# Optimization experiments

Hardware: AMD Instinct MI355X
Metric: run time of the kernel (lower is better)

Reference implementation:

```python
import jax, jax.numpy as jnp
import numpy as np

B, N, F, H1, H2, NC = 1024, 64, 1024, 256, 128, 128
ALPHA = 0.2   # LeakyReLU slope
BN_EPS = 1e-5


def setup_inputs() -> dict:
    key = jax.random.key(0)
    ks = jax.random.split(key, 20)
    d = {}
    d["x"] = jax.random.normal(ks[0], (B, 1, F), dtype=jnp.float32)
    d["neighbor"] = jax.random.normal(ks[1], (B, N, 1, F), dtype=jnp.float32)
    # GraphAttn layer 1 params
    d["W1"] = jax.random.normal(ks[2], (H1, F), dtype=jnp.float32) / np.sqrt(F)
    d["b1"] = jnp.zeros((H1,), dtype=jnp.float32)
    d["a11"] = jax.random.normal(ks[3], (H1,), dtype=jnp.float32) / np.sqrt(H1)
    d["a12"] = jax.random.normal(ks[4], (H1,), dtype=jnp.float32) / np.sqrt(H1)
    d["g1"] = jnp.ones((), dtype=jnp.float32)   # BatchNorm1d(1) weight (scalar)
    d["be1"] = jnp.zeros((), dtype=jnp.float32)  # BatchNorm1d(1) bias
    # GraphAttn layer 2 params
    d["W2"] = jax.random.normal(ks[5], (H2, H1), dtype=jnp.float32) / np.sqrt(H1)
    d["b2"] = jnp.zeros((H2,), dtype=jnp.float32)
    d["a21"] = jax.random.normal(ks[6], (H2,), dtype=jnp.float32) / np.sqrt(H2)
    d["a22"] = jax.random.normal(ks[7], (H2,), dtype=jnp.float32) / np.sqrt(H2)
    d["g2"] = jnp.ones((), dtype=jnp.float32)
    d["be2"] = jnp.zeros((), dtype=jnp.float32)
    # final classifier
    d["Wl"] = jax.random.normal(ks[8], (NC, H2), dtype=jnp.float32) / np.sqrt(H2)
    d["bl"] = jnp.zeros((NC,), dtype=jnp.float32)
    return d


def _l2norm_c(t):
    # torch nf.normalize default: p=2, dim=1 -> here the singleton channel axis (-2)
    n = jnp.sqrt(jnp.sum(t * t, axis=-2, keepdims=True))
    return t / jnp.maximum(n, 1e-12)


def _gat_layer(x, nb, W, b, a_self, a_nb):
    # x: [B,1,Fin], nb: [B,N,1,Fin]
    xh = jnp.einsum('bcf,hf->bch', x, W) + b        # [B,1,H]
    nbh = jnp.einsum('bncf,hf->bnch', nb, W) + b    # [B,N,1,H]
    # att1(x[i]) + att2(neighbor[i]) -> scores over N (C==1 squeezed)
    s = (jnp.einsum('bch,h->bc', xh, a_self)[:, None, :]
         + jnp.einsum('bnch,h->bnc', nbh, a_nb))[..., 0]   # [B,N]
    A = jax.nn.softmax(jax.nn.leaky_relu(s, ALPHA), axis=1)  # softmax over neighbors
    out = jnp.einsum('bn,bnch->bch', A, nbh)        # [B,1,H]
    return out, nbh


def _bn_relu(t, g, b, axes):
    # BatchNorm1d(1) in training mode: stats over all non-channel dims of the tensor
    m = jnp.mean(t, axis=axes, keepdims=True)
    v = jnp.mean(jnp.square(t - m), axis=axes, keepdims=True)
    return jax.nn.relu(g * (t - m) * jax.lax.rsqrt(v + BN_EPS) + b)


def reference(x, neighbor, W1, b1, a11, a12, g1, be1,
              W2, b2, a21, a22, g2, be2, Wl, bl):
    x = _l2norm_c(x)
    nb = _l2norm_c(neighbor)
    x, nb = _gat_layer(x, nb, W1, b1, a11, a12)
    # acvt1 applied to x [B,1,H1] (stats over B,H) and to each neighbor tensor
    # [N,1,H1] separately (per-sample stats -> axes (1,3) of [B,N,1,H1])
    x = _bn_relu(x, g1, be1, axes=(0, 2))
    nb = _bn_relu(nb, g1, be1, axes=(1, 3))
    x, nb = _gat_layer(x, nb, W2, b2, a21, a22)
    x = _bn_relu(x, g2, be2, axes=(0, 2))
    # Flatten -> Dropout(p=0) -> Linear
    logits = jnp.einsum('bh,ch->bc', x.reshape(x.shape[0], -1), Wl) + bl
    return logits
```

## Files before the change

kernel.cpp:

```cpp
#include <hip/hip_runtime.h>
#include <hip/hip_bf16.h>
#include <stdint.h>

#define B_    1024
#define N_    64
#define F_    1024
#define H1_   256
#define H2_   128
#define NC_   128
#define ALPHA 0.2f
#define BN_EPS 1e-5f

typedef __attribute__((ext_vector_type(4))) float  f32x4;
typedef __attribute__((ext_vector_type(8))) __bf16 bf16x8;
typedef __attribute__((ext_vector_type(4))) __bf16 bf16x4;

__device__ inline float sign_ref(float v) {
    float s = copysignf(1.0f, v);
    return (fabsf(v) >= 1e-12f) ? s : v * 1e12f;
}

__device__ __forceinline__ void gload_lds16(const void* g, void* l) {
    auto gp = reinterpret_cast<const __attribute__((address_space(1))) void*>(
        reinterpret_cast<uintptr_t>(g));
    auto lp = reinterpret_cast<__attribute__((address_space(3))) void*>(
        reinterpret_cast<uintptr_t>(l));
    __builtin_amdgcn_global_load_lds(gp, lp, 16, 0, 0);
}

__device__ inline float blk_reduce(float v, float* buf) {
    #pragma unroll
    for (int o = 32; o > 0; o >>= 1) v += __shfl_xor(v, o, 64);
    __syncthreads();
    const int wave = threadIdx.x >> 6, lane = threadIdx.x & 63;
    if (lane == 0) buf[wave] = v;
    __syncthreads();
    float r = 0.f;
    if (threadIdx.x == 0) {
        const int nw = blockDim.x >> 6;
        for (int i = 0; i < nw; ++i) r += buf[i];
    }
    return r;
}

__global__ __launch_bounds__(256) void k_prep(
    const float* __restrict__ W1, const float* __restrict__ W2,
    const float* __restrict__ b1, const float* __restrict__ a11,
    const float* __restrict__ a12, const float* __restrict__ b2,
    const float* __restrict__ a21, const float* __restrict__ a22,
    __bf16* __restrict__ W1f, __bf16* __restrict__ W2b,
    float* __restrict__ w1a, float* __restrict__ w2a,
    float* __restrict__ w2a22, float* __restrict__ cscal)
{
    __shared__ float rbuf[8];
    const int blk = blockIdx.x, tid = threadIdx.x;
    if (blk < 256) {
        const int h = blk, k0 = tid * 4;
        float4 v = *(const float4*)(W1 + h * F_ + k0);
        bf16x4 p = { (__bf16)v.x, (__bf16)v.y, (__bf16)v.z, (__bf16)v.w };
        const int kc = k0 >> 5, kq = (k0 >> 3) & 3, j = k0 & 7;
        const int rbk = h >> 4, rowin = h & 15;
        *(bf16x4*)(W1f + (size_t)((kc * 16 + rbk) * 64 + kq * 16 + rowin) * 8 + j) = p;
    } else if (blk < 288) {
        const int i0 = (blk - 256) * 1024 + tid * 4;
        float4 v = *(const float4*)(W2 + i0);
        bf16x4 p = { (__bf16)v.x, (__bf16)v.y, (__bf16)v.z, (__bf16)v.w };
        *(bf16x4*)(W2b + i0) = p;
    } else if (blk < 292) {
        const int f = (blk - 288) * 256 + tid;
        float s1 = 0.f;
        #pragma unroll 8
        for (int h = 0; h < H1_; ++h) s1 += W1[h * F_ + f] * a11[h];
        w1a[f] = s1;
    } else if (blk == 292) {
        float s1 = 0.f, s2 = 0.f;
        #pragma unroll 8
        for (int h = 0; h < H2_; ++h) {
            const float w = W2[h * H1_ + tid];
            s1 += w * a21[h]; s2 += w * a22[h];
        }
        w2a[tid] = s1; w2a22[tid] = s2;
    } else {
        float v1 = b1[tid] * a11[tid];
        float v2 = (tid < H2_) ? b2[tid] * a21[tid] : 0.f;
        float v3 = (tid < H2_) ? b2[tid] * a22[tid] : 0.f;
        float r1 = blk_reduce(v1, rbuf);
        float r2 = blk_reduce(v2, rbuf);
        float r3 = blk_reduce(v3, rbuf);
        if (tid == 0) { cscal[0] = r1; cscal[1] = r2; cscal[2] = r3; }
    }
}

__global__ __launch_bounds__(256, 3) void k_gemm1(
    const float* __restrict__ A, const __bf16* __restrict__ Bw,
    const float* __restrict__ bias, __bf16* __restrict__ C,
    const float* __restrict__ x, const float* __restrict__ w1a,
    const float* __restrict__ a12, const float* __restrict__ w2a22,
    const float* __restrict__ cscal, const float* __restrict__ g1p,
    const float* __restrict__ be1p,
    float* __restrict__ out1, float* __restrict__ alpha1,
    float* __restrict__ beta1, float* __restrict__ psum1,
    float* __restrict__ psq1, float* __restrict__ spart)
{
    constexpr int K = F_;
    constexpr int LDA = 72;
    __shared__ __attribute__((aligned(16))) char smem[64 * 256 * 2];
    __bf16* As0 = (__bf16*)smem;
    __bf16* As1 = As0 + 64 * LDA;
    __bf16* Cs  = (__bf16*)smem;
    __shared__ float a12s[H1_];
    __shared__ float w2a22s[H1_];
    __shared__ float sv[N_];
    __shared__ float rbuf[8];
    __shared__ float fscal[4];

    const int tid = threadIdx.x;
    const int wave = tid >> 6, lane = tid & 63;
    const int rowin = lane & 15, kq = lane >> 4;
    const size_t b = blockIdx.x;

    {
        const float* xb = x + b * F_;
        float p0 = 0.f;
        #pragma unroll
        for (int i = 0; i < 4; ++i)
            p0 += sign_ref(xb[tid + i * 256]) * w1a[tid + i * 256];
        a12s[tid] = a12[tid]; w2a22s[tid] = w2a22[tid];
        float r0 = blk_reduce(p0, rbuf);
        if (tid == 0) fscal[0] = r0 + cscal[0];
    }

    f32x4 acc[4][4] = {};

    const int cqA = tid & 15, r0A = tid >> 4;
    const float* Abase = A + b * (size_t)64 * K + cqA * 4;

    auto mfma_phase = [&](const __bf16* buf, int kc0) {
        #pragma unroll
        for (int ks = 0; ks < 2; ++ks) {
            bf16x8 af[4], bv[4];
            #pragma unroll
            for (int mi = 0; mi < 4; ++mi)
                af[mi] = *(const bf16x8*)&buf[(mi * 16 + rowin) * LDA + ks * 32 + kq * 8];
            #pragma unroll
            for (int ni = 0; ni < 4; ++ni)
                bv[ni] = ((const bf16x8*)Bw)[((kc0 + ks) * 16 + wave * 4 + ni) * 64 + lane];
            #pragma unroll
            for (int mi = 0; mi < 4; ++mi)
                #pragma unroll
                for (int ni = 0; ni < 4; ++ni)
                    acc[mi][ni] = __builtin_amdgcn_mfma_f32_16x16x32_bf16(
                        af[mi], bv[ni], acc[mi][ni], 0, 0, 0);
        }
    };
    auto stage = [&](__bf16* buf, const float4* av) {
        #pragma unroll
        for (int rr = 0; rr < 4; ++rr) {
            const float4 v = av[rr];
            bf16x4 p = { (__bf16)sign_ref(v.x), (__bf16)sign_ref(v.y),
                         (__bf16)sign_ref(v.z), (__bf16)sign_ref(v.w) };
            *(bf16x4*)&buf[(r0A + rr * 16) * LDA + cqA * 4] = p;
        }
    };

    float4 avA[4], avB[4];
    #pragma unroll
    for (int rr = 0; rr < 4; ++rr)
        avA[rr] = *(const float4*)(Abase + (size_t)(r0A + rr * 16) * K);

    for (int kk = 0; kk < 8; ++kk) {
        const int k0 = kk * 128;
        #pragma unroll
        for (int rr = 0; rr < 4; ++rr)
            avB[rr] = *(const float4*)(Abase + (size_t)(r0A + rr * 16) * K + k0 + 64);
        stage(As0, avA);
        asm volatile("s_waitcnt lgkmcnt(0)" ::: "memory");
        __builtin_amdgcn_s_barrier();
        __builtin_amdgcn_sched_barrier(0);
        mfma_phase(As0, kk * 4);
        if (kk < 7) {
            #pragma unroll
            for (int rr = 0; rr < 4; ++rr)
                avA[rr] = *(const float4*)(Abase + (size_t)(r0A + rr * 16) * K + k0 + 128);
        }
        stage(As1, avB);
        asm volatile("s_waitcnt lgkmcnt(0)" ::: "memory");
        __builtin_amdgcn_s_barrier();
        __builtin_amdgcn_sched_barrier(0);
        mfma_phase(As1, kk * 4 + 2);
    }
    __syncthreads();

    const int cr0 = (lane >> 4) * 4, cc = lane & 15;
    #pragma unroll
    for (int ni = 0; ni < 4; ++ni) {
        const int col = wave * 64 + ni * 16 + cc;
        const float bs = bias[col];
        #pragma unroll
        for (int mi = 0; mi < 4; ++mi)
            #pragma unroll
            for (int i = 0; i < 4; ++i)
                Cs[(mi * 16 + cr0 + i) * 256 + col] = (__bf16)(acc[mi][ni][i] + bs);
    }
    __syncthreads();
    #pragma unroll
    for (int it = 0; it < 8; ++it) {
        const int s = it * 256 + tid;
        *(bf16x8*)(C + (b * 64 + (s >> 5)) * 256 + (s & 31) * 8) =
            *(const bf16x8*)&Cs[s * 8];
    }
    {
        const int n = tid >> 2, q = tid & 3;
        float p = 0.f;
        for (int i = 0; i < 64; ++i) {
            const int h = q * 64 + ((i + tid) & 63);
            p += (float)Cs[n * 256 + h] * a12s[h];
        }
        p += __shfl_xor(p, 1); p += __shfl_xor(p, 2);
        if (q == 0) { float s = fscal[0] + p; sv[n] = s > 0.f ? s : ALPHA * s; }
    }
    __syncthreads();
    if (tid < 64) {
        float s = sv[tid], m = s;
        #pragma unroll
        for (int o = 1; o < 64; o <<= 1) m = fmaxf(m, __shfl_xor(m, o));
        float e = __expf(s - m), t = e;
        #pragma unroll
        for (int o = 1; o < 64; o <<= 1) t += __shfl_xor(t, o);
        sv[tid] = e / t;
    }
    __syncthreads();
    float o1 = 0.f, ss = 0.f, sq = 0.f;
    for (int n2 = 0; n2 < N_; ++n2) {
        const float v = (float)Cs[n2 * 256 + tid];
        o1 += sv[n2] * v; ss += v; sq += v * v;
    }
    out1[b * H1_ + tid] = o1;
    {
        const float rs = blk_reduce(ss, rbuf);
        const float rq = blk_reduce(sq, rbuf);
        if (tid == 0) {
            const float inv = 1.f / (float)(N_ * H1_);
            const float mean = rs * inv, var = rq * inv - mean * mean;
            const float a = (*g1p) * rsqrtf(var + BN_EPS);
            const float bb = (*be1p) - a * mean;
            alpha1[b] = a; beta1[b] = bb;
            fscal[2] = a; fscal[3] = bb;
        }
        const float rsx = blk_reduce(o1, rbuf);
        const float rqx = blk_reduce(o1 * o1, rbuf);
        if (tid == 0) { psum1[b] = rsx; psq1[b] = rqx; }
    }
    __syncthreads();
    {
        const float al_ = fscal[2], be_ = fscal[3];
        const int n = tid >> 2, q = tid & 3;
        float p = 0.f;
        for (int i = 0; i < 64; ++i) {
            const int h = q * 64 + ((i + tid) & 63);
            const float v = (float)Cs[n * 256 + h];
            p += fmaxf(fmaf(al_, v, be_), 0.f) * w2a22s[h];
        }
        p += __shfl_xor(p, 1); p += __shfl_xor(p, 2);
        if (q == 0) spart[b * N_ + n] = p;
    }
}

__global__ __launch_bounds__(256) void k_back(
    const __bf16* __restrict__ nbh1, const float* __restrict__ out1,
    const float* __restrict__ alpha1, const float* __restrict__ beta1,
    const float* __restrict__ psum1, const float* __restrict__ psq1,
    const float* __restrict__ g1p, const float* __restrict__ be1p,
    const float* __restrict__ w2a, const float* __restrict__ spart,
    const float* __restrict__ cscal, const __bf16* __restrict__ W2b,
    const float* __restrict__ b2,
    float* __restrict__ out2, float* __restrict__ psum2,
    float* __restrict__ psq2)
{
    __shared__ __attribute__((aligned(16))) __bf16 tile[N_ * H1_];
    __shared__ float w2as[H1_];
    __shared__ float sv[N_];
    __shared__ float g2s[H1_ + 8];
    __shared__ float hpart[H2_];
    __shared__ float rbuf[8];
    __shared__ float scal[3];

    const int b = blockIdx.x, tid = threadIdx.x;

    const __bf16* src = nbh1 + (size_t)b * N_ * H1_;
    #pragma unroll
    for (int it = 0; it < 8; ++it)
        gload_lds16(src + (it * 256 + tid) * 8, tile + (it * 256 + tid) * 8);
    w2as[tid] = w2a[tid];
    const float o1 = out1[(size_t)b * H1_ + tid];
    const float al = alpha1[b], be = beta1[b];

    {
        float s = 0.f, q = 0.f;
        for (int i = tid; i < B_; i += 256) { s += psum1[i]; q += psq1[i]; }
        const float gs = blk_reduce(s, rbuf);
        const float gq = blk_reduce(q, rbuf);
        if (tid == 0) {
            const float n = (float)(B_ * H1_);
            const float mean = gs / n, var = gq / n - mean * mean;
            const float a = (*g1p) * rsqrtf(var + BN_EPS);
            scal[0] = a; scal[1] = (*be1p) - a * mean;
        }
    }
    __syncthreads();

    {
        const float x2 = fmaxf(fmaf(scal[0], o1, scal[1]), 0.f);
        const float r = blk_reduce(x2 * w2as[tid], rbuf);
        if (tid == 0) scal[2] = r + cscal[1] + cscal[2];
    }
    __syncthreads();

    if (tid < 64) {
        float s = scal[2] + spart[(size_t)b * N_ + tid];
        s = s > 0.f ? s : ALPHA * s;
        float m = s;
        #pragma unroll
        for (int o = 1; o < 64; o <<= 1) m = fmaxf(m, __shfl_xor(m, o));
        float e = __expf(s - m), t = e;
        #pragma unroll
        for (int o = 1; o < 64; o <<= 1) t += __shfl_xor(t, o);
        sv[tid] = e / t;
    }
    __syncthreads();

    {
        float g = 0.f;
        for (int n2 = 0; n2 < N_; ++n2) {
            const float v = (float)tile[n2 * H1_ + tid];
            g += sv[n2] * fmaxf(fmaf(al, v, be), 0.f);
        }
        g2s[tid + (tid >> 5)] = g;
    }
    __syncthreads();

    #pragma unroll 4
    for (int j = 0; j < 16; ++j) {
        const int idx = j * 256 + tid;
        const int h = idx >> 5, k8 = idx & 31;
        const bf16x8 w = ((const bf16x8*)W2b)[idx];
        float p = 0.f;
        #pragma unroll
        for (int i = 0; i < 8; ++i) {
            const int k = k8 * 8 + i;
            p += (float)w[i] * g2s[k + (k >> 5)];
        }
        p += __shfl_xor(p, 1); p += __shfl_xor(p, 2); p += __shfl_xor(p, 4);
        p += __shfl_xor(p, 8); p += __shfl_xor(p, 16);
        if ((tid & 31) == 0) hpart[h] = p;
    }
    __syncthreads();
    {
        float o2 = 0.f;
        if (tid < H2_) o2 = hpart[tid] + b2[tid];
        const float rs2 = blk_reduce(o2, rbuf);
        const float rq2 = blk_reduce(o2 * o2, rbuf);
        if (tid < H2_) out2[(size_t)b * H2_ + tid] = o2;
        if (tid == 0) { psum2[b] = rs2; psq2[b] = rq2; }
    }
}

__global__ __launch_bounds__(128) void k_fin(
    const float* __restrict__ out2, const float* __restrict__ psum2,
    const float* __restrict__ psq2, const float* __restrict__ g2p,
    const float* __restrict__ be2p, const float* __restrict__ Wl,
    const float* __restrict__ bl, float* __restrict__ logits)
{
    __shared__ float xr[H2_];
    __shared__ float Ws[NC_][H2_ + 1];
    __shared__ float axbx[2];
    __shared__ float rbuf[8];
    const int b = blockIdx.x, tid = threadIdx.x;
    {
        float s = 0.f, q = 0.f;
        for (int i = tid; i < B_; i += 128) { s += psum2[i]; q += psq2[i]; }
        const float gs = blk_reduce(s, rbuf);
        const float gq = blk_reduce(q, rbuf);
        if (tid == 0) {
            const float n = (float)(B_ * H2_);
            const float mean = gs / n, var = gq / n - mean * mean;
            const float a = (*g2p) * rsqrtf(var + BN_EPS);
            axbx[0] = a; axbx[1] = (*be2p) - a * mean;
        }
    }
    for (int i = tid; i < NC_ * H2_ / 4; i += 128) {
        float4 v = ((const float4*)Wl)[i];
        const int r = i >> 5, c = (i & 31) * 4;
        Ws[r][c] = v.x; Ws[r][c + 1] = v.y; Ws[r][c + 2] = v.z; Ws[r][c + 3] = v.w;
    }
    __syncthreads();
    xr[tid] = fmaxf(fmaf(axbx[0], out2[(size_t)b * H2_ + tid], axbx[1]), 0.f);
    __syncthreads();
    float acc = bl[tid];
    #pragma unroll 4
    for (int h = 0; h < H2_; ++h) acc += xr[h] * Ws[tid][h];
    logits[(size_t)b * NC_ + tid] = acc;
}

extern "C" void kernel_launch(void* const* d_in, const int* in_sizes, int n_in,
                              void* d_out, int out_size, void* d_ws, size_t ws_size,
                              hipStream_t stream)
{
    const float* x   = (const float*)d_in[0];
    const float* nb  = (const float*)d_in[1];
    const float* W1  = (const float*)d_in[2];
    const float* b1  = (const float*)d_in[3];
    const float* a11 = (const float*)d_in[4];
    const float* a12 = (const float*)d_in[5];
    const float* g1  = (const float*)d_in[6];
    const float* be1 = (const float*)d_in[7];
    const float* W2  = (const float*)d_in[8];
    const float* b2  = (const float*)d_in[9];
    const float* a21 = (const float*)d_in[10];
    const float* a22 = (const float*)d_in[11];
    const float* g2  = (const float*)d_in[12];
    const float* be2 = (const float*)d_in[13];
    const float* Wl  = (const float*)d_in[14];
    const float* bl  = (const float*)d_in[15];
    float* logits = (float*)d_out;

    size_t off = 0;
    auto alc = [&](size_t bytes) {
        void* p = (char*)d_ws + off;
        off = (off + bytes + 255) & ~(size_t)255;
        return p;
    };
    __bf16* W1f   = (__bf16*)alc((size_t)H1_ * F_ * 2);
    __bf16* W2b   = (__bf16*)alc((size_t)H2_ * H1_ * 2);
    float* w1a    = (float*)alc(F_ * 4);
    float* w2a    = (float*)alc(H1_ * 4);
    float* w2a22  = (float*)alc(H1_ * 4);
    float* cscal  = (float*)alc(3 * 4);
    float* alpha1 = (float*)alc(B_ * 4);
    float* beta1  = (float*)alc(B_ * 4);
    float* psum1  = (float*)alc(B_ * 4);
    float* psq1   = (float*)alc(B_ * 4);
    float* psum2  = (float*)alc(B_ * 4);
    float* psq2   = (float*)alc(B_ * 4);
    float* spart  = (float*)alc((size_t)B_ * N_ * 4);
    float* out1   = (float*)alc((size_t)B_ * H1_ * 4);
    float* out2   = (float*)alc((size_t)B_ * H2_ * 4);
    __bf16* nbh1  = (__bf16*)alc((size_t)B_ * N_ * H1_ * 2);

    k_prep<<<294, 256, 0, stream>>>(W1, W2, b1, a11, a12, b2, a21, a22,
                                    W1f, W2b, w1a, w2a, w2a22, cscal);
    k_gemm1<<<B_, 256, 0, stream>>>(
        nb, W1f, b1, nbh1, x, w1a, a12, w2a22, cscal, g1, be1,
        out1, alpha1, beta1, psum1, psq1, spart);
    k_back<<<B_, 256, 0, stream>>>(nbh1, out1, alpha1, beta1, psum1, psq1,
                                   g1, be1, w2a, spart, cscal, W2b, b2,
                                   out2, psum2, psq2);
    k_fin<<<B_, 128, 0, stream>>>(out2, psum2, psq2, g2, be2, Wl, bl, logits);
}
```

Baseline: 493.4 us.

## Load A fragments directly from global into registers, dropping LDS staging in gemm1

The GEMM1 main loop no longer stages the normalized neighbor tile through double-buffered LDS with barriers. Each wave now reads its own A fragments straight from global memory, converts them to bf16 in registers, and feeds them to MFMA. This removes the LDS writes, the barriers and the waitcnt synchronization. In exchange, every wave re-reads the same A rows from global memory, which is a 4x redundancy that L1/L2 must absorb. Launch bounds drop from 3 to 2 blocks per SM, giving the compiler more registers.

Result: slower. 574.6 us (+16.5%).

```diff
diff --git a/kernel.cpp b/kernel.cpp
--- a/kernel.cpp
+++ b/kernel.cpp
@@ -91,7 +91,7 @@
     }
 }
 
-__global__ __launch_bounds__(256, 3) void k_gemm1(
+__global__ __launch_bounds__(256, 2) void k_gemm1(
     const float* __restrict__ A, const __bf16* __restrict__ Bw,
     const float* __restrict__ bias, __bf16* __restrict__ C,
     const float* __restrict__ x, const float* __restrict__ w1a,
@@ -103,11 +103,7 @@
     float* __restrict__ psq1, float* __restrict__ spart)
 {
     constexpr int K = F_;
-    constexpr int LDA = 72;
-    __shared__ __attribute__((aligned(16))) char smem[64 * 256 * 2];
-    __bf16* As0 = (__bf16*)smem;
-    __bf16* As1 = As0 + 64 * LDA;
-    __bf16* Cs  = (__bf16*)smem;
+    __shared__ __attribute__((aligned(16))) __bf16 Cs[64 * 256];
     __shared__ float a12s[H1_];
     __shared__ float w2a22s[H1_];
     __shared__ float sv[N_];
@@ -131,65 +127,35 @@
     }
 
     f32x4 acc[4][4] = {};
-
-    const int cqA = tid & 15, r0A = tid >> 4;
-    const float* Abase = A + b * (size_t)64 * K + cqA * 4;
-
-    auto mfma_phase = [&](const __bf16* buf, int kc0) {
-        #pragma unroll
-        for (int ks = 0; ks < 2; ++ks) {
-            bf16x8 af[4], bv[4];
-            #pragma unroll
-            for (int mi = 0; mi < 4; ++mi)
-                af[mi] = *(const bf16x8*)&buf[(mi * 16 + rowin) * LDA + ks * 32 + kq * 8];
+    const float* Ar = A + (b * 64 + rowin) * (size_t)K + kq * 8;
+    const bf16x8* Bv = (const bf16x8*)Bw;
+
+    #pragma unroll 2
+    for (int kc = 0; kc < 32; ++kc) {
+        bf16x8 bv[4];
+        #pragma unroll
+        for (int ni = 0; ni < 4; ++ni)
+            bv[ni] = Bv[(size_t)(kc * 16 + wave * 4 + ni) * 64 + lane];
+        bf16x8 af[4];
+        #pragma unroll
+        for (int mi = 0; mi < 4; ++mi) {
+            const float* p = Ar + (size_t)(mi * 16) * K + kc * 32;
+            const float4 v0 = *(const float4*)p;
+            const float4 v1 = *(const float4*)(p + 4);
+            bf16x8 t;
+            t[0] = (__bf16)sign_ref(v0.x); t[1] = (__bf16)sign_ref(v0.y);
+            t[2] = (__bf16)sign_ref(v0.z); t[3] = (__bf16)sign_ref(v0.w);
+            t[4] = (__bf16)sign_ref(v1.x); t[5] = (__bf16)sign_ref(v1.y);
+            t[6] = (__bf16)sign_ref(v1.z); t[7] = (__bf16)sign_ref(v1.w);
+            af[mi] = t;
+        }
+        #pragma unroll
+        for (int mi = 0; mi < 4; ++mi)
             #pragma unroll
             for (int ni = 0; ni < 4; ++ni)
-                bv[ni] = ((const bf16x8*)Bw)[((kc0 + ks) * 16 + wave * 4 + ni) * 64 + lane];
-            #pragma unroll
-            for (int mi = 0; mi < 4; ++mi)
-                #pragma unroll
-                for (int ni = 0; ni < 4; ++ni)
-                    acc[mi][ni] = __builtin_amdgcn_mfma_f32_16x16x32_bf16(
-                        af[mi], bv[ni], acc[mi][ni], 0, 0, 0);
-        }
-    };
-    auto stage = [&](__bf16* buf, const float4* av) {
-        #pragma unroll
-        for (int rr = 0; rr < 4; ++rr) {
-            const float4 v = av[rr];
-            bf16x4 p = { (__bf16)sign_ref(v.x), (__bf16)sign_ref(v.y),
-                         (__bf16)sign_ref(v.z), (__bf16)sign_ref(v.w) };
-            *(bf16x4*)&buf[(r0A + rr * 16) * LDA + cqA * 4] = p;
-        }
-    };
-
-    float4 avA[4], avB[4];
-    #pragma unroll
-    for (int rr = 0; rr < 4; ++rr)
-        avA[rr] = *(const float4*)(Abase + (size_t)(r0A + rr * 16) * K);
-
-    for (int kk = 0; kk < 8; ++kk) {
-        const int k0 = kk * 128;
-        #pragma unroll
-        for (int rr = 0; rr < 4; ++rr)
-            avB[rr] = *(const float4*)(Abase + (size_t)(r0A + rr * 16) * K + k0 + 64);
-        stage(As0, avA);
-        asm volatile("s_waitcnt lgkmcnt(0)" ::: "memory");
-        __builtin_amdgcn_s_barrier();
-        __builtin_amdgcn_sched_barrier(0);
-        mfma_phase(As0, kk * 4);
-        if (kk < 7) {
-            #pragma unroll
-            for (int rr = 0; rr < 4; ++rr)
-                avA[rr] = *(const float4*)(Abase + (size_t)(r0A + rr * 16) * K + k0 + 128);
-        }
-        stage(As1, avB);
-        asm volatile("s_waitcnt lgkmcnt(0)" ::: "memory");
-        __builtin_amdgcn_s_barrier();
-        __builtin_amdgcn_sched_barrier(0);
-        mfma_phase(As1, kk * 4 + 2);
-    }
-    __syncthreads();
+                acc[mi][ni] = __builtin_amdgcn_mfma_f32_16x16x32_bf16(
+                    af[mi], bv[ni], acc[mi][ni], 0, 0, 0);
+    }
 
     const int cr0 = (lane >> 4) * 4, cc = lane & 15;
     #pragma unroll
```
